# Performance work log

Hardware: AMD Instinct MI355X
Metric: run time of the kernel (lower is better)

## Reference

```python
import jax, jax.numpy as jnp
import numpy as np
import math

# Static module config (matches init_kwargs)
C = 1.0            # ball curvature parameter c
IN_C, OUT_C = 512, 512
K, PAD = 3, 1
T, B = 2048, 16
EPS = 1e-15
RC = math.sqrt(C)

def _beta(a, b):
    return math.exp(math.lgamma(a) + math.lgamma(b) - math.lgamma(a + b))

BETA_NI = _beta(IN_C / 2.0, 0.5)            # beta(n_i/2, 1/2)
BETA_N = _beta(IN_C * K / 2.0, 0.5)         # beta(n/2, 1/2)
BETA_RATIO = BETA_N / BETA_NI
PROJ_EPS = 4e-3                              # geoopt float32 projection eps


def logmap0(y):
    # y in Poincare ball -> tangent at origin
    yn = jnp.clip(jnp.linalg.norm(y, axis=-1, keepdims=True), EPS, None)
    arg = jnp.clip(RC * yn, None, 1.0 - 1e-7)
    return y * (jnp.arctanh(arg) / (RC * yn))


def expmap0(u):
    un = jnp.clip(jnp.linalg.norm(u, axis=-1, keepdims=True), EPS, None)
    return jnp.tanh(RC * un) * u / (RC * un)


def project(x):
    maxnorm = (1.0 - PROJ_EPS) / RC
    norm = jnp.clip(jnp.linalg.norm(x, axis=-1, keepdims=True), EPS, None)
    return x * jnp.where(norm > maxnorm, maxnorm / norm, 1.0)


def poincare_linear(x, w_g, w_unit, b):
    # unidirectional Poincare MLR (geoopt_plusplus)
    rcx = RC * x                                             # [T,B,K*Cin]
    cx2 = jnp.sum(rcx * rcx, axis=-1, keepdims=True)         # [T,B,1]
    drcr = 2.0 * RC * b                                      # [Cout]
    num = 2.0 * jnp.einsum('tbi,io->tbo', rcx, w_unit) * jnp.cosh(drcr) \
          - (1.0 + cx2) * jnp.sinh(drcr)
    y = (2.0 * w_g / RC) * jnp.arcsinh(num / jnp.clip(1.0 - cx2, EPS, None))
    y = jnp.sinh(RC * y) / RC
    denom = 1.0 + jnp.sqrt(1.0 + C * jnp.sum(y * y, axis=-1, keepdims=True))
    return project(y / denom)


def setup_inputs() -> dict:
    key = jax.random.key(0)
    k1, k2, k3 = jax.random.split(key, 3)
    # points strictly inside the unit ball: ||x|| < 0.7
    v = jax.random.normal(k1, (T, B, IN_C), dtype=jnp.float32)
    vn = jnp.linalg.norm(v, axis=-1, keepdims=True)
    x = v / (1.0 + vn) * 0.7
    std = (2.0 * IN_C * K * OUT_C) ** -0.5
    w = jax.random.normal(k2, (K * IN_C, OUT_C), dtype=jnp.float32) * std
    weight_g = jnp.clip(jnp.linalg.norm(w, axis=0), 1e-15, None)   # [Cout]
    weight_v = w / weight_g                                        # [K*Cin, Cout]
    bias = jnp.zeros((OUT_C,), dtype=jnp.float32)
    return {"x": x, "weight_g": weight_g, "weight_v": weight_v, "bias": bias}


def reference(x, weight_g, weight_v, bias):
    u = logmap0(x) * BETA_RATIO                 # tangent space, rescaled
    u = jnp.pad(u, ((PAD, PAD), (0, 0), (0, 0)))
    olen = u.shape[0] - K + 1
    # im2col over time: [olen, B, K*Cin]
    u = jnp.concatenate([u[k:k + olen] for k in range(K)], axis=-1)
    xh = expmap0(u)
    w_unit = weight_v / jnp.clip(jnp.linalg.norm(weight_v, axis=0), EPS, None)
    return poincare_linear(xh, weight_g, w_unit, bias)
```

## Files before the change

### kernel.cpp

```cpp
#include <hip/hip_runtime.h>
#include <cstdint>
#include <cmath>

typedef unsigned short u16;
typedef short bf16x8 __attribute__((ext_vector_type(8)));
typedef float f32x4 __attribute__((ext_vector_type(4)));

#define T_DIM 2048
#define B_DIM 16
#define CIN 512
#define COUT 512
#define KIN 1536
#define NROWS (T_DIM * B_DIM)
#define UROWS ((T_DIM + 2) * B_DIM)

#define NS 48

#define LOG2E 1.44269504088896f
#define LN2   0.69314718055995f

__device__ __forceinline__ float fast_exp2(float x) {
#if __has_builtin(__builtin_amdgcn_exp2f)
  return __builtin_amdgcn_exp2f(x);
#else
  return __builtin_exp2f(x);
#endif
}
__device__ __forceinline__ float fast_log2(float x) {
#if __has_builtin(__builtin_amdgcn_logf)
  return __builtin_amdgcn_logf(x);
#else
  return __builtin_log2f(x);
#endif
}
__device__ __forceinline__ float fast_rcp(float x) {
  return __builtin_amdgcn_rcpf(x);
}

__device__ __forceinline__ u16 f2bf(float f) {
  unsigned u = __builtin_bit_cast(unsigned, f);
  u = (u + 0x7FFFu + ((u >> 16) & 1u)) >> 16;
  return (u16)u;
}

typedef __attribute__((address_space(3))) unsigned int as3u32;
typedef __attribute__((address_space(1))) unsigned int as1u32;

__device__ __forceinline__ void gload16(const u16* g, const u16* lds) {
#if __has_builtin(__builtin_amdgcn_global_load_lds)
  __builtin_amdgcn_global_load_lds((as1u32*)(uintptr_t)g,
                                   (as3u32*)(unsigned)(uintptr_t)lds, 16, 0, 0);
#else
  unsigned lane = __lane_id();
  ((uint4*)lds)[lane] = *(const uint4*)g;
#endif
}

__global__ __launch_bounds__(256) void k_colnorm(const float* __restrict__ wv,
                                                 float* __restrict__ partial) {
  int o = blockIdx.x * 256 + threadIdx.x;
  int r0 = blockIdx.y * 64;
  float s = 0.f;
#pragma unroll 8
  for (int r = 0; r < 64; ++r) {
    float v = wv[(size_t)(r0 + r) * COUT + o];
    s += v * v;
  }
  partial[(size_t)blockIdx.y * COUT + o] = s;
}

__global__ __launch_bounds__(256) void k_fin(const float* __restrict__ partial,
                                             float* __restrict__ invn) {
  int o = blockIdx.x * 256 + threadIdx.x;
  float s = 0.f;
#pragma unroll
  for (int j = 0; j < KIN / 64; ++j) s += partial[(size_t)j * COUT + o];
  invn[o] = 1.f / fmaxf(sqrtf(s), 1e-15f);
}

__global__ void k_chsh(const float* __restrict__ bias, float* __restrict__ ch,
                       float* __restrict__ sh) {
  int o = blockIdx.x * blockDim.x + threadIdx.x;
  if (o < COUT) {
    float d = 2.f * bias[o];
    float e = fast_exp2(d * LOG2E);
    float ie = fast_rcp(e);
    ch[o] = 0.5f * (e + ie);
    sh[o] = 0.5f * (e - ie);
  }
}

__global__ void k_wt(const float* __restrict__ wv, const float* __restrict__ invn,
                     u16* __restrict__ wt) {
  __shared__ float tile[64][65];
  int i0 = blockIdx.x * 64;
  int o0 = blockIdx.y * 64;
  int tx = threadIdx.x & 63, ty = threadIdx.x >> 6;
  for (int r = ty; r < 64; r += 4)
    tile[r][tx] = wv[(size_t)(i0 + r) * COUT + o0 + tx];
  __syncthreads();
  for (int r = ty; r < 64; r += 4) {
    float inv = invn[o0 + r];
    wt[(size_t)(o0 + r) * KIN + i0 + tx] = f2bf(tile[tx][r] * inv);
  }
}

__global__ void k_logmap(const float* __restrict__ x, u16* __restrict__ U,
                         float* __restrict__ nsq, float beta_ratio) {
  int row = blockIdx.x;
  int t = row >> 4;
  int lane = threadIdx.x;
  uint4* urow = (uint4*)(U + (size_t)row * CIN);
  if (t == 0 || t == T_DIM + 1) {
    uint4 z; z.x = z.y = z.z = z.w = 0u;
    urow[lane] = z;
    if (lane == 0) nsq[row] = 0.f;
    return;
  }
  const float4* xr = (const float4*)(x + (size_t)(row - 16) * CIN);
  float4 a = xr[lane * 2];
  float4 b = xr[lane * 2 + 1];
  float s = a.x*a.x + a.y*a.y + a.z*a.z + a.w*a.w
          + b.x*b.x + b.y*b.y + b.z*b.z + b.w*b.w;
#pragma unroll
  for (int d = 1; d < 64; d <<= 1) s += __shfl_xor(s, d);
  float r = sqrtf(s);
  float yn = fmaxf(r, 1e-15f);
  float arg = fminf(yn, 1.0f - 1e-7f);
  float at = 0.5f * LN2 * fast_log2((1.f + arg) * fast_rcp(1.f - arg));
  float f = at / yn * beta_ratio;
  union { u16 h[8]; uint4 v; } pk;
  pk.h[0] = f2bf(a.x * f); pk.h[1] = f2bf(a.y * f);
  pk.h[2] = f2bf(a.z * f); pk.h[3] = f2bf(a.w * f);
  pk.h[4] = f2bf(b.x * f); pk.h[5] = f2bf(b.y * f);
  pk.h[6] = f2bf(b.z * f); pk.h[7] = f2bf(b.w * f);
  urow[lane] = pk.v;
  if (lane == 0) nsq[row] = s * f * f;
}

__global__ __launch_bounds__(512, 2) void k_gemm(const u16* __restrict__ U,
                                                 const u16* __restrict__ WT,
                                                 float* __restrict__ out) {
  __shared__ u16 lA[4][256 * 32];
  __shared__ u16 lB[4][256 * 32];
  int bid = blockIdx.x;
  int wgid = (bid & 7) * 32 + (bid >> 3);
  int bm = wgid >> 1, bn = wgid & 1;
  int tid = threadIdx.x;
  int lane = tid & 63;
  int wid = tid >> 6;
  int wr = wid >> 2, wc = wid & 3;
  int lr = lane & 15;
  int pcA = (((lane >> 4) ^ ((lr >> 1) & 3)) << 3);
  int srow0 = tid >> 2;
  int cir = tid & 3;

  f32x4 acc[8][4] = {};

  auto STG_A = [&](int s, int p) {
    int seg = s >> 4;
    int c0 = (s & 15) << 5;
#pragma unroll
    for (int r = 0; r < 2; ++r) {
      int row = r * 128 + srow0;
      int sc = cir ^ ((row >> 1) & 3);
      gload16(U + (size_t)(bm * 256 + seg * 16 + row) * 512 + c0 + sc * 8,
              &lA[p][(r * 128 + wid * 16) * 32]);
    }
  };
  auto STG_B = [&](int s, int p) {
#pragma unroll
    for (int r = 0; r < 2; ++r) {
      int row = r * 128 + srow0;
      int sc = cir ^ ((row >> 1) & 3);
      gload16(WT + (size_t)(bn * 256 + row) * KIN + s * 32 + sc * 8,
              &lB[p][(r * 128 + wid * 16) * 32]);
    }
  };

  STG_A(0, 0); STG_B(0, 0);
  STG_A(1, 1); STG_B(1, 1);
  STG_A(2, 2); STG_B(2, 2);

  for (int s = 0; s < NS; ++s) {
    int b = s & 3, pb = (s + 3) & 3;
    if (s < NS - 3) STG_A(s + 3, pb);
    if (s < NS - 3)      asm volatile("s_waitcnt vmcnt(10)" ::: "memory");
    else if (s == NS - 3) asm volatile("s_waitcnt vmcnt(8)" ::: "memory");
    else if (s == NS - 2) asm volatile("s_waitcnt vmcnt(4)" ::: "memory");
    else                  asm volatile("s_waitcnt vmcnt(0)" ::: "memory");
    asm volatile("s_barrier" ::: "memory");
    const u16* pA = &lA[b][(wr * 128 + lr) * 32 + pcA];
    const u16* pB = &lB[b][(wc * 64 + lr) * 32 + pcA];
    bf16x8 af0[4], af1[4], bfr[4];
#pragma unroll
    for (int i = 0; i < 4; ++i) af0[i] = *(const bf16x8*)(pA + i * 512);
#pragma unroll
    for (int i = 0; i < 4; ++i) bfr[i] = *(const bf16x8*)(pB + i * 512);
    __builtin_amdgcn_s_setprio(1);
#pragma unroll
    for (int mi = 0; mi < 4; ++mi)
#pragma unroll
      for (int ni = 0; ni < 4; ++ni)
        acc[mi][ni] = __builtin_amdgcn_mfma_f32_16x16x32_bf16(
            af0[mi], bfr[ni], acc[mi][ni], 0, 0, 0);
    __builtin_amdgcn_s_setprio(0);
    asm volatile("s_barrier" ::: "memory");
    if (s < NS - 3) STG_B(s + 3, pb);
#pragma unroll
    for (int i = 0; i < 4; ++i) af1[i] = *(const bf16x8*)(pA + (64 + i * 16) * 32);
    __builtin_amdgcn_s_setprio(1);
#pragma unroll
    for (int mi = 0; mi < 4; ++mi)
#pragma unroll
      for (int ni = 0; ni < 4; ++ni)
        acc[4 + mi][ni] = __builtin_amdgcn_mfma_f32_16x16x32_bf16(
            af1[mi], bfr[ni], acc[4 + mi][ni], 0, 0, 0);
    __builtin_amdgcn_s_setprio(0);
    asm volatile("s_waitcnt lgkmcnt(0)" ::: "memory");
    asm volatile("s_barrier" ::: "memory");
  }

  int orow = bm * 256 + wr * 128 + ((lane >> 4) << 2);
  int ocol = bn * 256 + wc * 64 + lr;
#pragma unroll
  for (int mi = 0; mi < 8; ++mi)
#pragma unroll
    for (int ni = 0; ni < 4; ++ni)
#pragma unroll
      for (int j = 0; j < 4; ++j)
        out[(size_t)(orow + mi * 16 + j) * COUT + (ocol + ni * 16)] = acc[mi][ni][j];
}

__global__ __launch_bounds__(128) void k_epi(float* __restrict__ out,
                                             const float* __restrict__ nsq,
                                             const float* __restrict__ wg,
                                             const float* __restrict__ chv,
                                             const float* __restrict__ shv) {
  int m = blockIdx.x;
  int tid = threadIdx.x;
  int lane = tid & 63, wv_ = tid >> 6;
  float un2 = nsq[m] + nsq[m + 16] + nsq[m + 32];
  float un = sqrtf(un2);
  float unc = fmaxf(un, 1e-15f);
  float e2 = fast_exp2(unc * (2.f * LOG2E));
  float th = (e2 - 1.f) * fast_rcp(e2 + 1.f);
  float sxp = th * fast_rcp(unc);
  float cx2 = sxp * sxp * un2;
  float iden = fast_rcp(fmaxf(1.f - cx2, 1e-15f));

  float4 dv = ((const float4*)(out + (size_t)m * COUT))[tid];
  float4 gv = ((const float4*)wg)[tid];
  float4 cv = ((const float4*)chv)[tid];
  float4 sv = ((const float4*)shv)[tid];
  float dot[4] = {dv.x, dv.y, dv.z, dv.w};
  float gvr[4] = {gv.x, gv.y, gv.z, gv.w};
  float chr[4] = {cv.x, cv.y, cv.z, cv.w};
  float shr[4] = {sv.x, sv.y, sv.z, sv.w};
  float y[4];
  float opc = 1.f + cx2;
#pragma unroll
  for (int e = 0; e < 4; ++e) {
    float num = 2.f * (sxp * dot[e]) * chr[e] - opc * shr[e];
    float z = num * iden;
    float w = z + sqrtf(fmaf(z, z, 1.f));
    float l = fast_log2(w);
    float E = fast_exp2((2.f * gvr[e]) * l);
    y[e] = 0.5f * (E - fast_rcp(E));
  }
  float ssl = y[0]*y[0] + y[1]*y[1] + y[2]*y[2] + y[3]*y[3];
#pragma unroll
  for (int d = 1; d < 64; d <<= 1) ssl += __shfl_xor(ssl, d);
  __shared__ float red[2];
  if (lane == 0) red[wv_] = ssl;
  __syncthreads();
  float ss = red[0] + red[1];
  float denom = 1.f + sqrtf(1.f + ss);
  float idn = 1.f / denom;
  float nrm = fmaxf(sqrtf(ss) * idn, 1e-15f);
  float maxn = 1.0f - 4e-3f;
  float scale = (nrm > maxn) ? (maxn / nrm) : 1.f;
  scale *= idn;
  float4 ov;
  ov.x = y[0] * scale;
  ov.y = y[1] * scale;
  ov.z = y[2] * scale;
  ov.w = y[3] * scale;
  ((float4*)(out + (size_t)m * COUT))[tid] = ov;
}

extern "C" void kernel_launch(void* const* d_in, const int* in_sizes, int n_in,
                              void* d_out, int out_size, void* d_ws, size_t ws_size,
                              hipStream_t stream) {
  const float* x    = (const float*)d_in[0];
  const float* wg   = (const float*)d_in[1];
  const float* wv   = (const float*)d_in[2];
  const float* bias = (const float*)d_in[3];
  float* out = (float*)d_out;

  char* ws = (char*)d_ws;
  u16*   U    = (u16*)(ws);
  float* NSQ  = (float*)(ws + 33587200);
  u16*   WT   = (u16*)(ws + 33718400);
  float* INVN = (float*)(ws + 35291264);
  float* CH   = (float*)(ws + 35293312);
  float* SH   = (float*)(ws + 35295360);
  float* PART = (float*)(ws + 35297408);

  double lb = (lgamma(768.0) + lgamma(0.5) - lgamma(768.5))
            - (lgamma(256.0) + lgamma(0.5) - lgamma(256.5));
  float beta_ratio = (float)exp(lb);

  k_colnorm<<<dim3(COUT / 256, KIN / 64), 256, 0, stream>>>(wv, PART);
  k_fin<<<COUT / 256, 256, 0, stream>>>(PART, INVN);
  k_chsh<<<COUT / 128, 128, 0, stream>>>(bias, CH, SH);
  k_wt<<<dim3(KIN / 64, COUT / 64), 256, 0, stream>>>(wv, INVN, WT);
  k_logmap<<<UROWS, 64, 0, stream>>>(x, U, NSQ, beta_ratio);
  k_gemm<<<(NROWS / 256) * (COUT / 256), 512, 0, stream>>>(U, WT, out);
  k_epi<<<NROWS, 128, 0, stream>>>(out, NSQ, wg, CH, SH);
}
```

Baseline: 120.6 us.

## Restructure GEMM mainloop into 64-wide K tiles with staggered half-tile prefetch

Replaces the 4-stage ring of 32-wide K slices with a double-buffered layout of 64-wide K tiles, each split into two halves. Global-to-LDS loads for the next halves are interleaved between the four MFMA phases per tile, with finer barrier and waitcnt placement, so the loads overlap compute more evenly. The goal is to hide memory latency with fewer wait points per K step. In exchange there are more barriers per iteration and the prefetch distance is shallower, which could expose latency; the buffer-reuse timing is also subtle and hard to get right.

```diff
diff --git a/kernel.cpp b/kernel.cpp
--- a/kernel.cpp
+++ b/kernel.cpp
@@ -14,7 +14,7 @@
 #define NROWS (T_DIM * B_DIM)
 #define UROWS ((T_DIM + 2) * B_DIM)
 
-#define NS 48
+#define NTILES 24
 
 #define LOG2E 1.44269504088896f
 #define LN2   0.69314718055995f
@@ -141,8 +141,8 @@
 __global__ __launch_bounds__(512, 2) void k_gemm(const u16* __restrict__ U,
                                                  const u16* __restrict__ WT,
                                                  float* __restrict__ out) {
-  __shared__ u16 lA[4][256 * 32];
-  __shared__ u16 lB[4][256 * 32];
+  __shared__ u16 lA[2][2][8192];
+  __shared__ u16 lB[2][2][8192];
   int bid = blockIdx.x;
   int wgid = (bid & 7) * 32 + (bid >> 3);
   int bm = wgid >> 1, bn = wgid & 1;
@@ -151,73 +151,104 @@
   int wid = tid >> 6;
   int wr = wid >> 2, wc = wid & 3;
   int lr = lane & 15;
-  int pcA = (((lane >> 4) ^ ((lr >> 1) & 3)) << 3);
-  int srow0 = tid >> 2;
-  int cir = tid & 3;
+  int srow = tid >> 2;
+  int sc = (tid & 3) ^ ((tid >> 3) & 3);
+  int cSwz = ((lane >> 4) ^ ((lr >> 1) & 3)) << 3;
 
   f32x4 acc[8][4] = {};
 
-  auto STG_A = [&](int s, int p) {
-    int seg = s >> 4;
-    int c0 = (s & 15) << 5;
-#pragma unroll
-    for (int r = 0; r < 2; ++r) {
-      int row = r * 128 + srow0;
-      int sc = cir ^ ((row >> 1) & 3);
-      gload16(U + (size_t)(bm * 256 + seg * 16 + row) * 512 + c0 + sc * 8,
-              &lA[p][(r * 128 + wid * 16) * 32]);
-    }
+  auto stgA = [&](int tt, int h) {
+    int ks32 = tt * 2 + h;
+    int seg = ks32 >> 4;
+    int c0 = (ks32 & 15) << 5;
+    const u16* g = U + (size_t)(bm * 256 + seg * 16 + srow) * 512 + c0 + sc * 8;
+    const u16* d = &lA[tt & 1][h][wid * 512];
+    gload16(g, d);
+    gload16(g + (size_t)128 * 512, d + 4096);
   };
-  auto STG_B = [&](int s, int p) {
-#pragma unroll
-    for (int r = 0; r < 2; ++r) {
-      int row = r * 128 + srow0;
-      int sc = cir ^ ((row >> 1) & 3);
-      gload16(WT + (size_t)(bn * 256 + row) * KIN + s * 32 + sc * 8,
-              &lB[p][(r * 128 + wid * 16) * 32]);
-    }
+  auto stgB = [&](int tt, int h) {
+    int ks32 = tt * 2 + h;
+    const u16* g = WT + (size_t)(bn * 256 + srow) * KIN + ks32 * 32 + sc * 8;
+    const u16* d = &lB[tt & 1][h][wid * 512];
+    gload16(g, d);
+    gload16(g + (size_t)128 * KIN, d + 4096);
   };
 
-  STG_A(0, 0); STG_B(0, 0);
-  STG_A(1, 1); STG_B(1, 1);
-  STG_A(2, 2); STG_B(2, 2);
-
-  for (int s = 0; s < NS; ++s) {
-    int b = s & 3, pb = (s + 3) & 3;
-    if (s < NS - 3) STG_A(s + 3, pb);
-    if (s < NS - 3)      asm volatile("s_waitcnt vmcnt(10)" ::: "memory");
-    else if (s == NS - 3) asm volatile("s_waitcnt vmcnt(8)" ::: "memory");
-    else if (s == NS - 2) asm volatile("s_waitcnt vmcnt(4)" ::: "memory");
-    else                  asm volatile("s_waitcnt vmcnt(0)" ::: "memory");
-    asm volatile("s_barrier" ::: "memory");
-    const u16* pA = &lA[b][(wr * 128 + lr) * 32 + pcA];
-    const u16* pB = &lB[b][(wc * 64 + lr) * 32 + pcA];
-    bf16x8 af0[4], af1[4], bfr[4];
-#pragma unroll
-    for (int i = 0; i < 4; ++i) af0[i] = *(const bf16x8*)(pA + i * 512);
-#pragma unroll
-    for (int i = 0; i < 4; ++i) bfr[i] = *(const bf16x8*)(pB + i * 512);
+  stgA(0, 0); stgB(0, 0); stgA(0, 1); stgB(0, 1);
+  stgB(1, 0); stgA(1, 0); stgB(1, 1);
+  asm volatile("s_waitcnt vmcnt(6)" ::: "memory");
+  asm volatile("s_barrier" ::: "memory");
+
+  for (int t = 0; t < NTILES; ++t) {
+    int b = t & 1;
+    const u16* pA = &lA[b][0][(wr * 128 + lr) * 32 + cSwz];
+    const u16* pB = &lB[b][0][(wc * 64 + lr) * 32 + cSwz];
+    bf16x8 af[4], bf[4];
+
+#pragma unroll
+    for (int i = 0; i < 4; ++i) bf[i] = *(const bf16x8*)(pB + i * 512);
+#pragma unroll
+    for (int i = 0; i < 4; ++i) af[i] = *(const bf16x8*)(pA + i * 512);
+    if (t + 1 < NTILES) stgA(t + 1, 1);
+    asm volatile("s_barrier" ::: "memory");
+    asm volatile("s_waitcnt lgkmcnt(0)" ::: "memory");
     __builtin_amdgcn_s_setprio(1);
 #pragma unroll
     for (int mi = 0; mi < 4; ++mi)
 #pragma unroll
       for (int ni = 0; ni < 4; ++ni)
         acc[mi][ni] = __builtin_amdgcn_mfma_f32_16x16x32_bf16(
-            af0[mi], bfr[ni], acc[mi][ni], 0, 0, 0);
+            af[mi], bf[ni], acc[mi][ni], 0, 0, 0);
     __builtin_amdgcn_s_setprio(0);
     asm volatile("s_barrier" ::: "memory");
-    if (s < NS - 3) STG_B(s + 3, pb);
-#pragma unroll
-    for (int i = 0; i < 4; ++i) af1[i] = *(const bf16x8*)(pA + (64 + i * 16) * 32);
+
+#pragma unroll
+    for (int i = 0; i < 4; ++i) af[i] = *(const bf16x8*)(pA + 2048 + i * 512);
+    if (t + 2 < NTILES) stgB(t + 2, 0);
+    asm volatile("s_barrier" ::: "memory");
+    asm volatile("s_waitcnt lgkmcnt(0)" ::: "memory");
     __builtin_amdgcn_s_setprio(1);
 #pragma unroll
     for (int mi = 0; mi < 4; ++mi)
 #pragma unroll
       for (int ni = 0; ni < 4; ++ni)
         acc[4 + mi][ni] = __builtin_amdgcn_mfma_f32_16x16x32_bf16(
-            af1[mi], bfr[ni], acc[4 + mi][ni], 0, 0, 0);
+            af[mi], bf[ni], acc[4 + mi][ni], 0, 0, 0);
     __builtin_amdgcn_s_setprio(0);
+    asm volatile("s_barrier" ::: "memory");
+
+#pragma unroll
+    for (int i = 0; i < 4; ++i) bf[i] = *(const bf16x8*)(pB + 8192 + i * 512);
+#pragma unroll
+    for (int i = 0; i < 4; ++i) af[i] = *(const bf16x8*)(pA + 8192 + i * 512);
+    if (t + 2 < NTILES) stgA(t + 2, 0);
+    asm volatile("s_barrier" ::: "memory");
     asm volatile("s_waitcnt lgkmcnt(0)" ::: "memory");
+    __builtin_amdgcn_s_setprio(1);
+#pragma unroll
+    for (int mi = 0; mi < 4; ++mi)
+#pragma unroll
+      for (int ni = 0; ni < 4; ++ni)
+        acc[mi][ni] = __builtin_amdgcn_mfma_f32_16x16x32_bf16(
+            af[mi], bf[ni], acc[mi][ni], 0, 0, 0);
+    __builtin_amdgcn_s_setprio(0);
+    asm volatile("s_barrier" ::: "memory");
+
+#pragma unroll
+    for (int i = 0; i < 4; ++i) af[i] = *(const bf16x8*)(pA + 8192 + 2048 + i * 512);
+    if (t + 2 < NTILES) stgB(t + 2, 1);
+    if (t < NTILES - 2) asm volatile("s_waitcnt vmcnt(6)" ::: "memory");
+    else                asm volatile("s_waitcnt vmcnt(0)" ::: "memory");
+    asm volatile("s_barrier" ::: "memory");
+    asm volatile("s_waitcnt lgkmcnt(0)" ::: "memory");
+    __builtin_amdgcn_s_setprio(1);
+#pragma unroll
+    for (int mi = 0; mi < 4; ++mi)
+#pragma unroll
+      for (int ni = 0; ni < 4; ++ni)
+        acc[4 + mi][ni] = __builtin_amdgcn_mfma_f32_16x16x32_bf16(
+            af[mi], bf[ni], acc[4 + mi][ni], 0, 0, 0);
+    __builtin_amdgcn_s_setprio(0);
     asm volatile("s_barrier" ::: "memory");
   }
 
```

After: 118.1 us. 1.02x faster.
